# Performance work log

Measured on AMD Instinct MI355X. Metric: run time of the kernel, lower is better.

## Reference

```python
import jax, jax.numpy as jnp
import numpy as np

B, C, H, W = 4, 256, 64, 64
D = C // 8  # qk projection dim = 32


def setup_inputs() -> dict:
    key = jax.random.key(0)
    ks = jax.random.split(key, 10)
    s = 1.0 / np.sqrt(C)
    return {
        "semantic_map": jax.random.normal(ks[0], (B, C, H, W), jnp.float32),
        "structural_map": jax.random.normal(ks[1], (B, C, H, W), jnp.float32),
        "Wq": jax.random.normal(ks[2], (D, C), jnp.float32) * s,
        "bq": jax.random.normal(ks[3], (D,), jnp.float32) * 0.01,
        "Wk": jax.random.normal(ks[4], (D, C), jnp.float32) * s,
        "bk": jax.random.normal(ks[5], (D,), jnp.float32) * 0.01,
        "Wv": jax.random.normal(ks[6], (C, C), jnp.float32) * s,
        "bv": jax.random.normal(ks[7], (C,), jnp.float32) * 0.01,
        "gamma": jnp.zeros((1,), jnp.float32) + 0.5,  # nonzero so the attention path matters
    }


def reference(semantic_map, structural_map, Wq, bq, Wk, bk, Wv, bv, gamma):
    b, c, h, w = semantic_map.shape
    n = h * w
    # 1x1 convs == per-pixel linear projections
    q = jnp.einsum("bchw,dc->bdhw", semantic_map, Wq) + bq[None, :, None, None]
    k = jnp.einsum("bchw,dc->bdhw", structural_map, Wk) + bk[None, :, None, None]
    v = jnp.einsum("bchw,oc->bohw", structural_map, Wv) + bv[None, :, None, None]
    q = q.reshape(b, -1, n).transpose(0, 2, 1)  # (B, HW, D)
    k = k.reshape(b, -1, n)                     # (B, D, HW)
    v = v.reshape(b, c, n)                      # (B, C, HW)
    energy = jnp.einsum("bid,bdj->bij", q, k)   # (B, HW, HW)
    attention = jax.nn.softmax(energy, axis=-1)
    # out[b,c,i] = sum_j v[b,c,j] * attention[b,i,j]
    out = jnp.einsum("bcj,bij->bci", v, attention).reshape(b, c, h, w)
    return gamma * out + semantic_map
```

## Files before the change

### kernel.cpp

```cpp
#include <hip/hip_runtime.h>

#define B_   4
#define C_   256
#define N_   4096
#define D_   32
#define CP   264

typedef _Float16 half8  __attribute__((ext_vector_type(8)));
typedef _Float16 half4v __attribute__((ext_vector_type(4)));
typedef _Float16 half2v __attribute__((ext_vector_type(2)));
typedef float    f32x4  __attribute__((ext_vector_type(4)));

__global__ __launch_bounds__(256) void wcvt_kernel(
    const float* __restrict__ Wq, const float* __restrict__ Wk,
    const float* __restrict__ Wv, _Float16* __restrict__ Wh)
{
    const int idx = blockIdx.x * 256 + threadIdx.x;
    const int kk  = idx & 31;
    const int row = (idx >> 5) & 15;
    const int kc  = (idx >> 9) & 7;
    const int t   = idx >> 12;
    const int c   = kc*32 + kk;
    float v;
    if (t < 2)      v = Wq[(t*16 + row)*C_ + c];
    else if (t < 4) v = Wk[((t-2)*16 + row)*C_ + c];
    else            v = Wv[((t-4)*16 + row)*C_ + c];
    Wh[idx] = (_Float16)v;
}

__global__ __launch_bounds__(512, 2) void proj_kernel(
    const float* __restrict__ sem, const float* __restrict__ str,
    const _Float16* __restrict__ Wh,
    const float* __restrict__ bq, const float* __restrict__ bk,
    const float* __restrict__ bv,
    _Float16* __restrict__ Qh, _Float16* __restrict__ Kh, _Float16* __restrict__ Vh2)
{
    __shared__ __align__(16) _Float16 s_x[64 * CP];
    __shared__ __align__(16) _Float16 s_s[64 * CP];
    __shared__ __align__(16) _Float16 s_v[8][3][1024];

    const int bid = blockIdx.x;
    const int nt6 = bid & 63;
    const int b   = bid >> 6;
    const int n0  = nt6 * 64;
    const int tid = threadIdx.x;
    const int w    = tid >> 6;
    const int lane = tid & 63;
    const int quad = lane >> 4;
    const int l15  = lane & 15;

    const int cnt = (w < 4) ? 3 : 2;
    const int t0  = (w < 4) ? w*3 : 12 + (w-4)*2;

    f32x4 acc[3][4];
    #pragma unroll
    for (int i = 0; i < 3; ++i)
        #pragma unroll
        for (int j = 0; j < 4; ++j) { acc[i][j][0]=0.f; acc[i][j][1]=0.f; acc[i][j][2]=0.f; acc[i][j][3]=0.f; }

    const size_t xbase = (size_t)b * C_ * N_;

    #pragma unroll
    for (int r = 0; r < 4; ++r) {
        const int slot = r*512 + tid;
        const int nq = slot & 15;
        const int cp = slot >> 4;
        const float* p0 = str + xbase + (size_t)(2*cp) * N_ + n0 + nq*4;
        const float4 a4 = *(const float4*)p0;
        const float4 b4 = *(const float4*)(p0 + N_);
        #pragma unroll
        for (int t = 0; t < 4; ++t) {
            half2v hp; hp[0] = (_Float16)a4[t]; hp[1] = (_Float16)b4[t];
            *(half2v*)(s_x + (nq*4 + t)*CP + 2*cp) = hp;
        }
        const float* p1 = sem + xbase + (size_t)(2*cp) * N_ + n0 + nq*4;
        const float4 c4 = *(const float4*)p1;
        const float4 d4 = *(const float4*)(p1 + N_);
        #pragma unroll
        for (int t = 0; t < 4; ++t) {
            half2v hp; hp[0] = (_Float16)c4[t]; hp[1] = (_Float16)d4[t];
            *(half2v*)(s_s + (nq*4 + t)*CP + 2*cp) = hp;
        }
    }
    __syncthreads();

    auto afload = [&](half8 (&af)[3], int kc) {
        #pragma unroll
        for (int mi = 0; mi < 3; ++mi)
            if (mi < cnt)
                af[mi] = *(const half8*)(Wh + ((size_t)(((t0+mi)*8 + kc)*16 + l15))*32 + quad*8);
    };
    auto bload = [&](half8 (&bfr)[4], half8 (&sfr)[4], int kc) {
        #pragma unroll
        for (int nt = 0; nt < 4; ++nt)
            bfr[nt] = *(const half8*)(s_x + (nt*16 + l15)*CP + kc*32 + quad*8);
        if (w == 0) {
            #pragma unroll
            for (int nt = 0; nt < 4; ++nt)
                sfr[nt] = *(const half8*)(s_s + (nt*16 + l15)*CP + kc*32 + quad*8);
        }
    };
    auto domfma = [&](const half8 (&af)[3], const half8 (&bfr)[4], const half8 (&sfr)[4]) {
        #pragma unroll
        for (int mi = 0; mi < 3; ++mi) {
            if (mi >= cnt) break;
            const bool useS = (t0 + mi) < 2;
            #pragma unroll
            for (int nt = 0; nt < 4; ++nt)
                acc[mi][nt] = __builtin_amdgcn_mfma_f32_16x16x32_f16(
                                  af[mi], useS ? sfr[nt] : bfr[nt], acc[mi][nt], 0, 0, 0);
        }
    };

    half8 afA[3], afB[3];
    afload(afA, 0);
    #pragma unroll 1
    for (int kc2 = 0; kc2 < 4; ++kc2) {
        const int kc = kc2*2;
        half8 bfr[4], sfr[4];
        bload(bfr, sfr, kc);
        afload(afB, kc+1);
        domfma(afA, bfr, sfr);
        half8 bfr2[4], sfr2[4];
        bload(bfr2, sfr2, kc+1);
        if (kc2 < 3) afload(afA, kc+2);
        domfma(afB, bfr2, sfr2);
    }

    #pragma unroll
    for (int mi = 0; mi < 3; ++mi) {
        if (mi >= cnt) break;
        const int t = t0 + mi;
        if (t < 4) {
            const bool isq = (t < 2);
            const int  tt  = isq ? t : (t - 2);
            f32x4 b4 = *(const f32x4*)((isq ? bq : bk) + tt*16 + quad*4);
            _Float16* dst = isq ? Qh : Kh;
            const int dc  = tt*2 + (quad >> 1);
            const int off = (quad & 1) * 4;
            #pragma unroll
            for (int nt = 0; nt < 4; ++nt) {
                const int n = n0 + nt*16 + l15;
                f32x4 a = acc[mi][nt];
                half4v hq;
                hq[0]=(_Float16)(a[0]+b4[0]); hq[1]=(_Float16)(a[1]+b4[1]);
                hq[2]=(_Float16)(a[2]+b4[2]); hq[3]=(_Float16)(a[3]+b4[3]);
                *(half4v*)(dst + ((size_t)(b*4 + dc) * N_ + n) * 8 + off) = hq;
            }
        } else {
            const int ctg = t - 4;
            f32x4 b4 = *(const f32x4*)(bv + ctg*16 + quad*4);
            #pragma unroll
            for (int nt = 0; nt < 4; ++nt) {
                const int js = nt & 1;
                const int hb = nt >> 1;
                f32x4 a = acc[mi][nt];
                #pragma unroll
                for (int r = 0; r < 4; ++r)
                    s_v[w][mi][hb*512 + ((l15>>2)*16 + quad*4 + r)*8 + js*4 + (l15&3)]
                        = (_Float16)(a[r] + b4[r]);
            }
        }
    }
    {
        _Float16* vb = Vh2 + (size_t)b * (size_t)N_ * C_;
        const int jc2_0 = n0 >> 5;
        #pragma unroll
        for (int mi = 0; mi < 3; ++mi) {
            if (mi >= cnt) break;
            const int t = t0 + mi;
            if (t >= 4) {
                const int ctg = t - 4;
                #pragma unroll
                for (int hb = 0; hb < 2; ++hb) {
                    half8 vv = *(const half8*)(&s_v[w][mi][hb*512 + lane*8]);
                    *(half8*)(vb + (size_t)(jc2_0 + hb)*8192 + (size_t)ctg*512 + lane*8) = vv;
                }
            }
        }
    }
}

__global__ __launch_bounds__(256, 2) void flash_kernel(
    const _Float16* __restrict__ Qh, const _Float16* __restrict__ Kh,
    const _Float16* __restrict__ Vh2, const float* __restrict__ sem,
    const float* __restrict__ gma, float* __restrict__ out)
{
    __shared__ float s_mp[4*32];
    __shared__ float s_lp[4*32];
    __shared__ __align__(16) float s_red[4][64][32];

    const int bid = blockIdx.x;
    const int b   = bid >> 7;
    const int i0  = (bid & 127) * 32;
    const int tid = threadIdx.x;
    const int w    = tid >> 6;
    const int lane = tid & 63;
    const int quad = lane >> 4;
    const int l15  = lane & 15;
    const int wc   = w & 1;
    const int wj   = w >> 1;

    const _Float16* qk_base = Qh + (size_t)(b*4 + quad) * N_ * 8;
    const half8 qf0 = *(const half8*)(qk_base + (size_t)(i0 + l15) * 8);
    const half8 qf1 = *(const half8*)(qk_base + (size_t)(i0 + 16 + l15) * 8);

    const _Float16* klane = Kh + ((size_t)(b*4 + quad) * N_ + l15) * 8;
    const _Float16* vl    = Vh2 + (size_t)b * (size_t)N_ * C_
                            + (size_t)(wc*8) * 512 + (size_t)lane * 8;

    float mx0 = -3e38f, mx1 = -3e38f;
    {
        half8 kp[4], kn[4];
        auto kl4 = [&](half8 (&kf)[4], int j0) {
            #pragma unroll
            for (int js = 0; js < 4; ++js)
                kf[js] = *(const half8*)(klane + (size_t)(j0 + js*16) * 8);
        };
        auto p0step = [&](const half8 (&kf)[4], half8 (&kfn)[4], int j0, bool more) {
            if (more) kl4(kfn, j0 + 64);
            #pragma unroll
            for (int js = 0; js < 4; ++js) {
                f32x4 z; z[0]=0.f; z[1]=0.f; z[2]=0.f; z[3]=0.f;
                f32x4 s0 = __builtin_amdgcn_mfma_f32_16x16x32_f16(kf[js], qf0, z, 0, 0, 0);
                f32x4 s1 = __builtin_amdgcn_mfma_f32_16x16x32_f16(kf[js], qf1, z, 0, 0, 0);
                #pragma unroll
                for (int r = 0; r < 4; ++r) { mx0 = fmaxf(mx0, s0[r]); mx1 = fmaxf(mx1, s1[r]); }
            }
        };
        kl4(kp, w*1024);
        #pragma unroll 1
        for (int it2 = 0; it2 < 8; ++it2) {
            const int j0 = w*1024 + it2*128;
            p0step(kp, kn, j0, true);
            p0step(kn, kp, j0 + 64, it2 < 7);
        }
    }
    mx0 = fmaxf(mx0, __shfl_xor(mx0, 16)); mx0 = fmaxf(mx0, __shfl_xor(mx0, 32));
    mx1 = fmaxf(mx1, __shfl_xor(mx1, 16)); mx1 = fmaxf(mx1, __shfl_xor(mx1, 32));
    if (lane < 32) s_mp[w*32 + lane] = (lane < 16) ? mx0 : mx1;
    __syncthreads();
    float mf0 = -3e38f, mf1 = -3e38f;
    #pragma unroll
    for (int ww = 0; ww < 4; ++ww) {
        mf0 = fmaxf(mf0, s_mp[ww*32 + l15]);
        mf1 = fmaxf(mf1, s_mp[ww*32 + 16 + l15]);
    }

    f32x4 acc[8][2];
    #pragma unroll
    for (int ct = 0; ct < 8; ++ct)
        #pragma unroll
        for (int f = 0; f < 2; ++f) { acc[ct][f][0]=0.f; acc[ct][f][1]=0.f; acc[ct][f][2]=0.f; acc[ct][f][3]=0.f; }
    float l0 = 0.f, l1 = 0.f;

    half8 kA[2], kB[2], vA[8], vB[8];

    auto kl2 = [&](half8 (&kf)[2], int j0) {
        kf[0] = *(const half8*)(klane + (size_t)j0 * 8);
        kf[1] = *(const half8*)(klane + (size_t)(j0 + 16) * 8);
    };
    auto vl8 = [&](half8 (&vf)[8], int j0) {
        const _Float16* p = vl + (size_t)(j0 >> 5) * 8192;
        #pragma unroll
        for (int ct = 0; ct < 8; ++ct)
            vf[ct] = *(const half8*)(p + ct*512);
    };
    auto mkp = [](const f32x4& s, float mf, float& lacc) -> half4v {
        float e0 = __expf(s[0]-mf), e1 = __expf(s[1]-mf);
        float e2 = __expf(s[2]-mf), e3 = __expf(s[3]-mf);
        lacc += (e0+e1)+(e2+e3);
        half2v p01 = __builtin_bit_cast(half2v, __builtin_amdgcn_cvt_pkrtz(e0, e1));
        half2v p23 = __builtin_bit_cast(half2v, __builtin_amdgcn_cvt_pkrtz(e2, e3));
        return __builtin_shufflevector(p01, p23, 0, 1, 2, 3);
    };

    auto step = [&](const half8 (&kf)[2], const half8 (&vf)[8],
                    half8 (&kfn)[2], half8 (&vfn)[8], int j0, bool more) {
        f32x4 z; z[0]=0.f; z[1]=0.f; z[2]=0.f; z[3]=0.f;
        f32x4 sf0[2], sf1[2];
        #pragma unroll
        for (int js = 0; js < 2; ++js) {
            sf0[js] = __builtin_amdgcn_mfma_f32_16x16x32_f16(kf[js], qf0, z, 0, 0, 0);
            sf1[js] = __builtin_amdgcn_mfma_f32_16x16x32_f16(kf[js], qf1, z, 0, 0, 0);
        }
        if (more) {
            kl2(kfn, j0 + 32);
            vl8(vfn, j0 + 32);
        }
        half4v pa0 = mkp(sf0[0], mf0, l0);
        half4v pb0 = mkp(sf0[1], mf0, l0);
        half4v pa1 = mkp(sf1[0], mf1, l1);
        half4v pb1 = mkp(sf1[1], mf1, l1);
        half8 pcat0 = __builtin_shufflevector(pa0, pb0, 0, 1, 2, 3, 4, 5, 6, 7);
        half8 pcat1 = __builtin_shufflevector(pa1, pb1, 0, 1, 2, 3, 4, 5, 6, 7);
        __builtin_amdgcn_s_setprio(1);
        #pragma unroll
        for (int ct = 0; ct < 8; ++ct) {
            acc[ct][0] = __builtin_amdgcn_mfma_f32_16x16x32_f16(vf[ct], pcat0, acc[ct][0], 0, 0, 0);
            acc[ct][1] = __builtin_amdgcn_mfma_f32_16x16x32_f16(vf[ct], pcat1, acc[ct][1], 0, 0, 0);
        }
        __builtin_amdgcn_s_setprio(0);
    };

    const int jb = wj * 2048;
    kl2(kA, jb);
    vl8(vA, jb);
    #pragma unroll 1
    for (int s2 = 0; s2 < 32; ++s2) {
        const int j0 = jb + s2*64;
        step(kA, vA, kB, vB, j0, true);
        step(kB, vB, kA, vA, j0 + 32, s2 < 31);
    }

    l0 += __shfl_xor(l0, 16); l0 += __shfl_xor(l0, 32);
    l1 += __shfl_xor(l1, 16); l1 += __shfl_xor(l1, 32);
    if (lane < 32) s_lp[w*32 + lane] = (lane < 16) ? l0 : l1;

    const int kx = (lane & 7) << 2;
    if (wj == 0) {
        #pragma unroll
        for (int t2 = 0; t2 < 4; ++t2) {
            *(f32x4*)&s_red[w][lane][(t2*8)     ^ kx] = acc[4 + t2][0];
            *(f32x4*)&s_red[w][lane][(t2*8 + 4) ^ kx] = acc[4 + t2][1];
        }
    } else {
        #pragma unroll
        for (int t2 = 0; t2 < 4; ++t2) {
            *(f32x4*)&s_red[w][lane][(t2*8)     ^ kx] = acc[t2][0];
            *(f32x4*)&s_red[w][lane][(t2*8 + 4) ^ kx] = acc[t2][1];
        }
    }
    __syncthreads();

    const float lt0 = s_lp[wc*32 + l15]      + s_lp[64 + wc*32 + l15];
    const float lt1 = s_lp[wc*32 + 16 + l15] + s_lp[64 + wc*32 + 16 + l15];
    const float g = gma[0];
    const float sc0 = g / lt0, sc1 = g / lt1;
    const int wp = w ^ 2;

    if (wj == 0) {
        #pragma unroll
        for (int t2 = 0; t2 < 4; ++t2) {
            f32x4 r0 = *(const f32x4*)&s_red[wp][lane][(t2*8)     ^ kx];
            f32x4 r1 = *(const f32x4*)&s_red[wp][lane][(t2*8 + 4) ^ kx];
            r0 += acc[t2][0];
            r1 += acc[t2][1];
            const int cb0 = (wc*8 + t2)*16 + quad*4;
            #pragma unroll
            for (int r4 = 0; r4 < 4; ++r4) {
                const size_t idx = ((size_t)(b*C_ + cb0 + r4)) * N_ + i0 + l15;
                out[idx]      = r0[r4] * sc0 + sem[idx];
                out[idx + 16] = r1[r4] * sc1 + sem[idx + 16];
            }
        }
    } else {
        #pragma unroll
        for (int t2 = 0; t2 < 4; ++t2) {
            f32x4 r0 = *(const f32x4*)&s_red[wp][lane][(t2*8)     ^ kx];
            f32x4 r1 = *(const f32x4*)&s_red[wp][lane][(t2*8 + 4) ^ kx];
            r0 += acc[4 + t2][0];
            r1 += acc[4 + t2][1];
            const int cb0 = (wc*8 + 4 + t2)*16 + quad*4;
            #pragma unroll
            for (int r4 = 0; r4 < 4; ++r4) {
                const size_t idx = ((size_t)(b*C_ + cb0 + r4)) * N_ + i0 + l15;
                out[idx]      = r0[r4] * sc0 + sem[idx];
                out[idx + 16] = r1[r4] * sc1 + sem[idx + 16];
            }
        }
    }
}

extern "C" void kernel_launch(void* const* d_in, const int* in_sizes, int n_in,
                              void* d_out, int out_size, void* d_ws, size_t ws_size,
                              hipStream_t stream) {
    const float* sem = (const float*)d_in[0];
    const float* str = (const float*)d_in[1];
    const float* Wq  = (const float*)d_in[2];
    const float* bq  = (const float*)d_in[3];
    const float* Wk  = (const float*)d_in[4];
    const float* bk  = (const float*)d_in[5];
    const float* Wv  = (const float*)d_in[6];
    const float* bv  = (const float*)d_in[7];
    const float* gma = (const float*)d_in[8];
    float* out = (float*)d_out;

    _Float16* Qh  = (_Float16*)d_ws;
    _Float16* Kh  = Qh + (size_t)B_*N_*D_;
    _Float16* Vh2 = Kh + (size_t)B_*N_*D_;
    _Float16* Wh  = Vh2 + (size_t)B_*C_*N_;

    hipLaunchKernelGGL(wcvt_kernel, dim3(320), dim3(256), 0, stream, Wq, Wk, Wv, Wh);
    hipLaunchKernelGGL(proj_kernel, dim3(B_*(N_/64)), dim3(512), 0, stream,
                       sem, str, Wh, bq, bk, bv, Qh, Kh, Vh2);
    hipLaunchKernelGGL(flash_kernel, dim3(B_*(N_/32)), dim3(256), 0, stream,
                       Qh, Kh, Vh2, sem, gma, out);
}
```

Baseline: 157.1 us.

## Enlarge flash tile to 64 queries with 8 waves and XCD-aware block mapping

The attention kernel now processes 64 query rows per block using 512 threads. Each wave covers 64 channels instead of 128, so every V fragment is reused across four query tiles rather than two, which halves V and K traffic per query. Block indices are remapped so that blocks sharing a batch land on the same XCD, improving L2 reuse of K/V. The cost is fewer blocks (256) and a larger LDS footprint, which may lower occupancy and cover the CUs less evenly.

```diff
diff --git a/kernel.cpp b/kernel.cpp
--- a/kernel.cpp
+++ b/kernel.cpp
@@ -181,35 +181,40 @@
     }
 }
 
-__global__ __launch_bounds__(256, 2) void flash_kernel(
+__global__ __launch_bounds__(512, 2) void flash_kernel(
     const _Float16* __restrict__ Qh, const _Float16* __restrict__ Kh,
     const _Float16* __restrict__ Vh2, const float* __restrict__ sem,
     const float* __restrict__ gma, float* __restrict__ out)
 {
-    __shared__ float s_mp[4*32];
-    __shared__ float s_lp[4*32];
-    __shared__ __align__(16) float s_red[4][64][32];
-
-    const int bid = blockIdx.x;
-    const int b   = bid >> 7;
-    const int i0  = (bid & 127) * 32;
+    __shared__ float s_mp[8*64];
+    __shared__ float s_lp[8*64];
+    __shared__ __align__(16) float s_red[8][64][32];
+
+    const int g   = blockIdx.x;
+    const int xcd = g & 7;
+    const int b   = xcd >> 1;
+    const int i0  = ((xcd & 1)*32 + (g >> 3)) * 64;
     const int tid = threadIdx.x;
     const int w    = tid >> 6;
     const int lane = tid & 63;
     const int quad = lane >> 4;
     const int l15  = lane & 15;
-    const int wc   = w & 1;
-    const int wj   = w >> 1;
+    const int wc   = w >> 1;
+    const int wj   = w & 1;
 
     const _Float16* qk_base = Qh + (size_t)(b*4 + quad) * N_ * 8;
-    const half8 qf0 = *(const half8*)(qk_base + (size_t)(i0 + l15) * 8);
-    const half8 qf1 = *(const half8*)(qk_base + (size_t)(i0 + 16 + l15) * 8);
+    half8 qf[4];
+    #pragma unroll
+    for (int i = 0; i < 4; ++i)
+        qf[i] = *(const half8*)(qk_base + (size_t)(i0 + i*16 + l15) * 8);
 
     const _Float16* klane = Kh + ((size_t)(b*4 + quad) * N_ + l15) * 8;
     const _Float16* vl    = Vh2 + (size_t)b * (size_t)N_ * C_
-                            + (size_t)(wc*8) * 512 + (size_t)lane * 8;
-
-    float mx0 = -3e38f, mx1 = -3e38f;
+                            + (size_t)(wc*4) * 512 + (size_t)lane * 8;
+
+    float mx[4];
+    #pragma unroll
+    for (int i = 0; i < 4; ++i) mx[i] = -3e38f;
     {
         half8 kp[4], kn[4];
         auto kl4 = [&](half8 (&kf)[4], int j0) {
@@ -222,90 +227,102 @@
             #pragma unroll
             for (int js = 0; js < 4; ++js) {
                 f32x4 z; z[0]=0.f; z[1]=0.f; z[2]=0.f; z[3]=0.f;
-                f32x4 s0 = __builtin_amdgcn_mfma_f32_16x16x32_f16(kf[js], qf0, z, 0, 0, 0);
-                f32x4 s1 = __builtin_amdgcn_mfma_f32_16x16x32_f16(kf[js], qf1, z, 0, 0, 0);
                 #pragma unroll
-                for (int r = 0; r < 4; ++r) { mx0 = fmaxf(mx0, s0[r]); mx1 = fmaxf(mx1, s1[r]); }
+                for (int i = 0; i < 4; ++i) {
+                    f32x4 s = __builtin_amdgcn_mfma_f32_16x16x32_f16(kf[js], qf[i], z, 0, 0, 0);
+                    #pragma unroll
+                    for (int r = 0; r < 4; ++r) mx[i] = fmaxf(mx[i], s[r]);
+                }
             }
         };
-        kl4(kp, w*1024);
+        kl4(kp, w*512);
         #pragma unroll 1
-        for (int it2 = 0; it2 < 8; ++it2) {
-            const int j0 = w*1024 + it2*128;
+        for (int it2 = 0; it2 < 4; ++it2) {
+            const int j0 = w*512 + it2*128;
             p0step(kp, kn, j0, true);
-            p0step(kn, kp, j0 + 64, it2 < 7);
-        }
-    }
-    mx0 = fmaxf(mx0, __shfl_xor(mx0, 16)); mx0 = fmaxf(mx0, __shfl_xor(mx0, 32));
-    mx1 = fmaxf(mx1, __shfl_xor(mx1, 16)); mx1 = fmaxf(mx1, __shfl_xor(mx1, 32));
-    if (lane < 32) s_mp[w*32 + lane] = (lane < 16) ? mx0 : mx1;
+            p0step(kn, kp, j0 + 64, it2 < 3);
+        }
+    }
+    #pragma unroll
+    for (int i = 0; i < 4; ++i) {
+        mx[i] = fmaxf(mx[i], __shfl_xor(mx[i], 16));
+        mx[i] = fmaxf(mx[i], __shfl_xor(mx[i], 32));
+    }
+    {
+        const float mv = (lane < 16) ? mx[0] : (lane < 32) ? mx[1] : (lane < 48) ? mx[2] : mx[3];
+        s_mp[w*64 + lane] = mv;
+    }
     __syncthreads();
-    float mf0 = -3e38f, mf1 = -3e38f;
-    #pragma unroll
-    for (int ww = 0; ww < 4; ++ww) {
-        mf0 = fmaxf(mf0, s_mp[ww*32 + l15]);
-        mf1 = fmaxf(mf1, s_mp[ww*32 + 16 + l15]);
-    }
-
-    f32x4 acc[8][2];
-    #pragma unroll
-    for (int ct = 0; ct < 8; ++ct)
-        #pragma unroll
-        for (int f = 0; f < 2; ++f) { acc[ct][f][0]=0.f; acc[ct][f][1]=0.f; acc[ct][f][2]=0.f; acc[ct][f][3]=0.f; }
-    float l0 = 0.f, l1 = 0.f;
-
-    half8 kA[2], kB[2], vA[8], vB[8];
+    float mf[4];
+    #pragma unroll
+    for (int i = 0; i < 4; ++i) {
+        float m = -3e38f;
+        #pragma unroll
+        for (int ww = 0; ww < 8; ++ww) m = fmaxf(m, s_mp[ww*64 + i*16 + l15]);
+        mf[i] = m;
+    }
+
+    f32x4 acc[4][4];
+    #pragma unroll
+    for (int ct = 0; ct < 4; ++ct)
+        #pragma unroll
+        for (int i = 0; i < 4; ++i) { acc[ct][i][0]=0.f; acc[ct][i][1]=0.f; acc[ct][i][2]=0.f; acc[ct][i][3]=0.f; }
+    float l4[4] = {0.f, 0.f, 0.f, 0.f};
+
+    half8 kA[2], kB[2], vA[4], vB[4];
 
     auto kl2 = [&](half8 (&kf)[2], int j0) {
         kf[0] = *(const half8*)(klane + (size_t)j0 * 8);
         kf[1] = *(const half8*)(klane + (size_t)(j0 + 16) * 8);
     };
-    auto vl8 = [&](half8 (&vf)[8], int j0) {
+    auto vl4 = [&](half8 (&vf)[4], int j0) {
         const _Float16* p = vl + (size_t)(j0 >> 5) * 8192;
         #pragma unroll
-        for (int ct = 0; ct < 8; ++ct)
+        for (int ct = 0; ct < 4; ++ct)
             vf[ct] = *(const half8*)(p + ct*512);
     };
-    auto mkp = [](const f32x4& s, float mf, float& lacc) -> half4v {
-        float e0 = __expf(s[0]-mf), e1 = __expf(s[1]-mf);
-        float e2 = __expf(s[2]-mf), e3 = __expf(s[3]-mf);
+    auto mkp = [](const f32x4& s, float mfv, float& lacc) -> half4v {
+        float e0 = __expf(s[0]-mfv), e1 = __expf(s[1]-mfv);
+        float e2 = __expf(s[2]-mfv), e3 = __expf(s[3]-mfv);
         lacc += (e0+e1)+(e2+e3);
         half2v p01 = __builtin_bit_cast(half2v, __builtin_amdgcn_cvt_pkrtz(e0, e1));
         half2v p23 = __builtin_bit_cast(half2v, __builtin_amdgcn_cvt_pkrtz(e2, e3));
         return __builtin_shufflevector(p01, p23, 0, 1, 2, 3);
     };
 
-    auto step = [&](const half8 (&kf)[2], const half8 (&vf)[8],
-                    half8 (&kfn)[2], half8 (&vfn)[8], int j0, bool more) {
+    auto step = [&](const half8 (&kf)[2], const half8 (&vf)[4],
+                    half8 (&kfn)[2], half8 (&vfn)[4], int j0, bool more) {
         f32x4 z; z[0]=0.f; z[1]=0.f; z[2]=0.f; z[3]=0.f;
-        f32x4 sf0[2], sf1[2];
-        #pragma unroll
-        for (int js = 0; js < 2; ++js) {
-            sf0[js] = __builtin_amdgcn_mfma_f32_16x16x32_f16(kf[js], qf0, z, 0, 0, 0);
-            sf1[js] = __builtin_amdgcn_mfma_f32_16x16x32_f16(kf[js], qf1, z, 0, 0, 0);
-        }
+        f32x4 sf0[4], sf1[4];
+        #pragma unroll
+        for (int i = 0; i < 4; ++i)
+            sf0[i] = __builtin_amdgcn_mfma_f32_16x16x32_f16(kf[0], qf[i], z, 0, 0, 0);
+        #pragma unroll
+        for (int i = 0; i < 4; ++i)
+            sf1[i] = __builtin_amdgcn_mfma_f32_16x16x32_f16(kf[1], qf[i], z, 0, 0, 0);
         if (more) {
             kl2(kfn, j0 + 32);
-            vl8(vfn, j0 + 32);
-        }
-        half4v pa0 = mkp(sf0[0], mf0, l0);
-        half4v pb0 = mkp(sf0[1], mf0, l0);
-        half4v pa1 = mkp(sf1[0], mf1, l1);
-        half4v pb1 = mkp(sf1[1], mf1, l1);
-        half8 pcat0 = __builtin_shufflevector(pa0, pb0, 0, 1, 2, 3, 4, 5, 6, 7);
-        half8 pcat1 = __builtin_shufflevector(pa1, pb1, 0, 1, 2, 3, 4, 5, 6, 7);
+            vl4(vfn, j0 + 32);
+        }
+        half8 pcat[4];
+        #pragma unroll
+        for (int i = 0; i < 4; ++i) {
+            half4v pa = mkp(sf0[i], mf[i], l4[i]);
+            half4v pb = mkp(sf1[i], mf[i], l4[i]);
+            pcat[i] = __builtin_shufflevector(pa, pb, 0, 1, 2, 3, 4, 5, 6, 7);
+        }
         __builtin_amdgcn_s_setprio(1);
         #pragma unroll
-        for (int ct = 0; ct < 8; ++ct) {
-            acc[ct][0] = __builtin_amdgcn_mfma_f32_16x16x32_f16(vf[ct], pcat0, acc[ct][0], 0, 0, 0);
-            acc[ct][1] = __builtin_amdgcn_mfma_f32_16x16x32_f16(vf[ct], pcat1, acc[ct][1], 0, 0, 0);
-        }
+        for (int ct = 0; ct < 4; ++ct)
+            #pragma unroll
+            for (int i = 0; i < 4; ++i)
+                acc[ct][i] = __builtin_amdgcn_mfma_f32_16x16x32_f16(vf[ct], pcat[i], acc[ct][i], 0, 0, 0);
         __builtin_amdgcn_s_setprio(0);
     };
 
     const int jb = wj * 2048;
     kl2(kA, jb);
-    vl8(vA, jb);
+    vl4(vA, jb);
     #pragma unroll 1
     for (int s2 = 0; s2 < 32; ++s2) {
         const int j0 = jb + s2*64;
@@ -313,60 +330,48 @@
         step(kB, vB, kA, vA, j0 + 32, s2 < 31);
     }
 
-    l0 += __shfl_xor(l0, 16); l0 += __shfl_xor(l0, 32);
-    l1 += __shfl_xor(l1, 16); l1 += __shfl_xor(l1, 32);
-    if (lane < 32) s_lp[w*32 + lane] = (lane < 16) ? l0 : l1;
+    #pragma unroll
+    for (int i = 0; i < 4; ++i) {
+        l4[i] += __shfl_xor(l4[i], 16);
+        l4[i] += __shfl_xor(l4[i], 32);
+    }
+    {
+        const float lv = (lane < 16) ? l4[0] : (lane < 32) ? l4[1] : (lane < 48) ? l4[2] : l4[3];
+        s_lp[w*64 + lane] = lv;
+    }
 
     const int kx = (lane & 7) << 2;
-    if (wj == 0) {
-        #pragma unroll
-        for (int t2 = 0; t2 < 4; ++t2) {
-            *(f32x4*)&s_red[w][lane][(t2*8)     ^ kx] = acc[4 + t2][0];
-            *(f32x4*)&s_red[w][lane][(t2*8 + 4) ^ kx] = acc[4 + t2][1];
-        }
-    } else {
-        #pragma unroll
-        for (int t2 = 0; t2 < 4; ++t2) {
-            *(f32x4*)&s_red[w][lane][(t2*8)     ^ kx] = acc[t2][0];
-            *(f32x4*)&s_red[w][lane][(t2*8 + 4) ^ kx] = acc[t2][1];
-        }
-    }
+    const int cput = wj ? 0 : 2;
+    #pragma unroll
+    for (int t2 = 0; t2 < 2; ++t2)
+        #pragma unroll
+        for (int i = 0; i < 4; ++i)
+            *(f32x4*)&s_red[w][lane][(t2*16 + i*4) ^ kx] = acc[cput + t2][i];
     __syncthreads();
 
-    const float lt0 = s_lp[wc*32 + l15]      + s_lp[64 + wc*32 + l15];
-    const float lt1 = s_lp[wc*32 + 16 + l15] + s_lp[64 + wc*32 + 16 + l15];
-    const float g = gma[0];
-    const float sc0 = g / lt0, sc1 = g / lt1;
-    const int wp = w ^ 2;
-
-    if (wj == 0) {
-        #pragma unroll
-        for (int t2 = 0; t2 < 4; ++t2) {
-            f32x4 r0 = *(const f32x4*)&s_red[wp][lane][(t2*8)     ^ kx];
-            f32x4 r1 = *(const f32x4*)&s_red[wp][lane][(t2*8 + 4) ^ kx];
-            r0 += acc[t2][0];
-            r1 += acc[t2][1];
-            const int cb0 = (wc*8 + t2)*16 + quad*4;
+    float sc[4];
+    {
+        const float gv = gma[0];
+        #pragma unroll
+        for (int i = 0; i < 4; ++i) {
+            const float lt = s_lp[(w & ~1)*64 + 64*0 + i*16 + l15]
+                           + s_lp[((w & ~1) | 1)*64 + i*16 + l15];
+            sc[i] = gv / lt;
+        }
+    }
+    const int cown = wj ? 2 : 0;
+    #pragma unroll
+    for (int t2 = 0; t2 < 2; ++t2) {
+        #pragma unroll
+        for (int i = 0; i < 4; ++i) {
+            f32x4 r = acc[cown + t2][i];
+            f32x4 o = *(const f32x4*)&s_red[w ^ 1][lane][(t2*16 + i*4) ^ kx];
+            r[0]+=o[0]; r[1]+=o[1]; r[2]+=o[2]; r[3]+=o[3];
+            const int c0 = (wc*4 + cown + t2)*16 + quad*4;
             #pragma unroll
             for (int r4 = 0; r4 < 4; ++r4) {
-                const size_t idx = ((size_t)(b*C_ + cb0 + r4)) * N_ + i0 + l15;
-                out[idx]      = r0[r4] * sc0 + sem[idx];
-                out[idx + 16] = r1[r4] * sc1 + sem[idx + 16];
-            }
-        }
-    } else {
-        #pragma unroll
-        for (int t2 = 0; t2 < 4; ++t2) {
-            f32x4 r0 = *(const f32x4*)&s_red[wp][lane][(t2*8)     ^ kx];
-            f32x4 r1 = *(const f32x4*)&s_red[wp][lane][(t2*8 + 4) ^ kx];
-            r0 += acc[4 + t2][0];
-            r1 += acc[4 + t2][1];
-            const int cb0 = (wc*8 + 4 + t2)*16 + quad*4;
-            #pragma unroll
-            for (int r4 = 0; r4 < 4; ++r4) {
-                const size_t idx = ((size_t)(b*C_ + cb0 + r4)) * N_ + i0 + l15;
-                out[idx]      = r0[r4] * sc0 + sem[idx];
-                out[idx + 16] = r1[r4] * sc1 + sem[idx + 16];
+                const size_t idx = ((size_t)(b*C_ + c0 + r4)) * N_ + i0 + i*16 + l15;
+                out[idx] = r[r4] * sc[i] + sem[idx];
             }
         }
     }
@@ -394,6 +399,6 @@
     hipLaunchKernelGGL(wcvt_kernel, dim3(320), dim3(256), 0, stream, Wq, Wk, Wv, Wh);
     hipLaunchKernelGGL(proj_kernel, dim3(B_*(N_/64)), dim3(512), 0, stream,
                        sem, str, Wh, bq, bk, bv, Qh, Kh, Vh2);
-    hipLaunchKernelGGL(flash_kernel, dim3(B_*(N_/32)), dim3(256), 0, stream,
+    hipLaunchKernelGGL(flash_kernel, dim3(256), dim3(512), 0, stream,
                        Qh, Kh, Vh2, sem, gma, out);
 }
```

Measured after the change: 177.1 us. 1.13x slower.
